# Performance work log

Hardware: AMD Instinct MI355X
Metric: run time of the kernel (lower is better)

## Reference

```python
import jax, jax.numpy as jnp
import numpy as np

TEMP = 0.3  # softmax temperature used in load-balance loss


def setup_inputs() -> dict:
    key = jax.random.key(0)
    k1, k2 = jax.random.split(key)
    num_tokens, d_model, num_expert = 16384, 4096, 128
    inp = jax.random.normal(k1, (num_tokens, d_model), dtype=jnp.float32)
    wg = jax.random.normal(k2, (num_expert, d_model), dtype=jnp.float32) * (1.0 / np.sqrt(d_model))
    return {"inp": inp, "wg": wg, "top_k": 2}


def reference(inp, wg, top_k):
    # Gate logits: [T, E] = [T, D] @ [D, E]
    logits = jnp.einsum("td,ed->te", inp, wg)
    # Top-k selection + softmax over the k selected logits
    top_vals, top_idx = jax.lax.top_k(logits, top_k)  # [T, k]
    gate_score = jax.nn.softmax(top_vals, axis=-1)    # [T, k]
    # Load-balance loss (stored as self.loss in torch; returned here)
    T, E = logits.shape
    probs = jax.nn.softmax(logits / TEMP, axis=-1)    # [T, E]
    mask = jax.nn.one_hot(top_idx[:, 0], E, dtype=probs.dtype) * (E / T)
    me = jnp.sum(probs, axis=0)                       # [E]
    ce = jnp.sum(mask, axis=0)                        # [E]
    loss = jnp.sum(me * ce) / T
    return top_idx, gate_score, loss
```

## Files before the change

### kernel.cpp

```cpp
#include <hip/hip_runtime.h>

typedef _Float16 half8 __attribute__((ext_vector_type(8)));
typedef float floatx4 __attribute__((ext_vector_type(4)));

#define NTOK 16384
#define DM   4096
#define NE   128
#define MT   32
#define BK   64
#define KSPLIT 2
#define KHALF (DM / KSPLIT)
#define NITER (KHALF / BK)
#define NBLK_MAIN (NTOK / MT * KSPLIT)
#define ET   64
#define NBLK_EPI (NTOK / ET)
#define TEMP 0.3f
#define CSTRIDE 528
#define ABUF (8 * CSTRIDE)
#define BUFSZ (2 * ABUF)

__global__ void pack_b_kernel(const float* __restrict__ wg, _Float16* __restrict__ Bp) {
    int gtid = blockIdx.x * blockDim.x + threadIdx.x;
    int l  = gtid & 63;
    int tg = gtid >> 6;
    int g  = tg & 7;
    int kc = tg >> 3;
    const float* src = wg + (size_t)(g * 16 + (l & 15)) * DM + kc * 32 + (l >> 4) * 8;
    float4 v0 = *(const float4*)src;
    float4 v1 = *(const float4*)(src + 4);
    float f[8] = {v0.x, v0.y, v0.z, v0.w, v1.x, v1.y, v1.z, v1.w};
    half8 h1, h2;
#pragma unroll
    for (int j = 0; j < 8; j++) {
        h1[j] = (_Float16)f[j];
        h2[j] = (_Float16)((f[j] - (float)h1[j]) * 2048.0f);
    }
    char* dst = (char*)Bp + (size_t)tg * 2048 + l * 16;
    *(half8*)dst = h1;
    *(half8*)(dst + 1024) = h2;
}

__device__ __forceinline__ void stage_write(unsigned char* base, unsigned off,
                                            float4 v0, float4 v1) {
    float f[8] = {v0.x, v0.y, v0.z, v0.w, v1.x, v1.y, v1.z, v1.w};
    half8 h1, h2;
#pragma unroll
    for (int j = 0; j < 8; j++) {
        h1[j] = (_Float16)f[j];
        h2[j] = (_Float16)((f[j] - (float)h1[j]) * 2048.0f);
    }
    *(half8*)(base + off) = h1;
    *(half8*)(base + ABUF + off) = h2;
}

__launch_bounds__(256, 4)
__global__ void moe_gemm_kernel(const float* __restrict__ A,
                                const _Float16* __restrict__ Bp,
                                float* __restrict__ part) {
    __shared__ __align__(16) unsigned char smem[2 * BUFSZ];
    const int tid  = threadIdx.x;
    const int wave = tid >> 6;
    const int lane = tid & 63;
    const int quad = lane >> 4;
    const int lrow = lane & 15;
    const int half = blockIdx.x & 1;
    const int tok0 = (blockIdx.x >> 1) * MT;

    const int srow = tid >> 3;
    const int schunk = tid & 7;
    const float* aptr = A + (size_t)(tok0 + srow) * DM + half * KHALF + schunk * 8;
    const unsigned swoff = schunk * CSTRIDE + srow * 16;
    const unsigned aroff = quad * CSTRIDE + lrow * 16;

    const char* bB = (const char*)Bp + (size_t)half * (1u << 20) + (wave * 2) * 2048 + lane * 16;

    floatx4 accm[2][2], accc[2][2];
#pragma unroll
    for (int r = 0; r < 2; r++)
#pragma unroll
        for (int c = 0; c < 2; c++) {
            accm[r][c] = (floatx4){0.f, 0.f, 0.f, 0.f};
            accc[r][c] = (floatx4){0.f, 0.f, 0.f, 0.f};
        }

    {
        float4 v0 = *(const float4*)aptr;
        float4 v1 = *(const float4*)(aptr + 4);
        stage_write(smem, swoff, v0, v1);
    }
    __syncthreads();

    for (int it = 0; it < NITER; ++it) {
        float4 n0, n1;
        if (it < NITER - 1) {
            const float* p = aptr + (it + 1) * BK;
            n0 = *(const float4*)p;
            n1 = *(const float4*)(p + 4);
        }
        unsigned char* cb = smem + (it & 1) * BUFSZ;
        const char* bit = bB + (size_t)it * 32768;

#pragma unroll
        for (int ks = 0; ks < 2; ++ks) {
            half8 b1f[2], b2f[2], a1[2], a2[2];
#pragma unroll
            for (int c = 0; c < 2; c++) {
                b1f[c] = *(const half8*)(bit + ks * 16384 + c * 2048);
                b2f[c] = *(const half8*)(bit + ks * 16384 + c * 2048 + 1024);
            }
#pragma unroll
            for (int r = 0; r < 2; r++) {
                a1[r] = *(const half8*)(cb + ks * 2112 + r * 256 + aroff);
                a2[r] = *(const half8*)(cb + ABUF + ks * 2112 + r * 256 + aroff);
            }
#pragma unroll
            for (int r = 0; r < 2; r++)
#pragma unroll
                for (int c = 0; c < 2; c++) {
                    accm[r][c] = __builtin_amdgcn_mfma_f32_16x16x32_f16(a1[r], b1f[c], accm[r][c], 0, 0, 0);
                    accc[r][c] = __builtin_amdgcn_mfma_f32_16x16x32_f16(a1[r], b2f[c], accc[r][c], 0, 0, 0);
                    accc[r][c] = __builtin_amdgcn_mfma_f32_16x16x32_f16(a2[r], b1f[c], accc[r][c], 0, 0, 0);
                }
        }
        if (it < NITER - 1)
            stage_write(smem + ((it + 1) & 1) * BUFSZ, swoff, n0, n1);
        __syncthreads();
    }

    float* pbase = part + (size_t)half * NTOK * NE;
#pragma unroll
    for (int r = 0; r < 2; r++)
#pragma unroll
        for (int c = 0; c < 2; c++) {
            floatx4 v;
#pragma unroll
            for (int g = 0; g < 4; g++)
                v[g] = accm[r][c][g] + accc[r][c][g] * (1.0f / 2048.0f);
            int e = wave * 32 + c * 16 + lrow;
            int t = tok0 + r * 16 + quad * 4;
            *(floatx4*)(pbase + (size_t)e * NTOK + t) = v;
        }
}

__global__ void topk_kernel(const float* __restrict__ part,
                            float* __restrict__ out,
                            float* __restrict__ me_part,
                            float* __restrict__ ce_part) {
    __shared__ float LG[NE * 68];
    __shared__ float tmax[ET], tscale[ET];
    __shared__ int hist[NE];
    const int tid = threadIdx.x;
    const int t0  = blockIdx.x * ET;
    const float* p0 = part;
    const float* p1 = part + (size_t)NTOK * NE;

    {
        const int q = tid & 3;
#pragma unroll
        for (int pass = 0; pass < 2; pass++) {
            int e = (tid >> 2) + pass * 64;
            const float* r0 = p0 + (size_t)e * NTOK + t0 + q * 16;
            const float* r1 = p1 + (size_t)e * NTOK + t0 + q * 16;
            float* dst = LG + e * 68 + q * 16;
#pragma unroll
            for (int j = 0; j < 16; j += 4) {
                float4 a = *(const float4*)(r0 + j);
                float4 b = *(const float4*)(r1 + j);
                float4 s = {a.x + b.x, a.y + b.y, a.z + b.z, a.w + b.w};
                *(float4*)(dst + j) = s;
            }
        }
    }
    if (tid < NE) hist[tid] = 0;
    __syncthreads();

    if (tid < ET) {
        const int t = tid;
        float m1 = -1e30f, m2 = -1e30f;
        int i1 = 0, i2 = 0;
        for (int e = 0; e < NE; e++) {
            float v = LG[e * 68 + t];
            if (v > m1) { m2 = m1; i2 = i1; m1 = v; i1 = e; }
            else if (v > m2) { m2 = v; i2 = e; }
        }
        float s = 0.f;
        for (int e = 0; e < NE; e++)
            s += __expf((LG[e * 68 + t] - m1) * (1.0f / TEMP));
        tmax[t] = m1;
        tscale[t] = 1.0f / s;
        atomicAdd(&hist[i1], 1);

        const int tg = t0 + t;
        out[tg * 2 + 0] = (float)i1;
        out[tg * 2 + 1] = (float)i2;
        float d = __expf(m2 - m1);
        float g1 = 1.0f / (1.0f + d);
        out[2 * NTOK + tg * 2 + 0] = g1;
        out[2 * NTOK + tg * 2 + 1] = d * g1;
    }
    __syncthreads();

    if (tid < NE) {
        const int e = tid;
        float s = 0.f;
        for (int t = 0; t < ET; t++)
            s += __expf((LG[e * 68 + t] - tmax[t]) * (1.0f / TEMP)) * tscale[t];
        me_part[blockIdx.x * NE + e] = s;
        ce_part[blockIdx.x * NE + e] = (float)hist[e];
    }
}

__global__ void finalize_kernel(const float* __restrict__ mp, const float* __restrict__ cp,
                                float* __restrict__ out) {
    __shared__ float red[2 * 8 * 128];
    __shared__ float wsum[2];
    const int tid = threadIdx.x;
    const int e = tid & 127, seg = tid >> 7;
    float sm = 0.f, sc = 0.f;
    for (int b = seg; b < NBLK_EPI; b += 8) {
        sm += mp[b * NE + e];
        sc += cp[b * NE + e];
    }
    red[seg * 128 + e] = sm;
    red[1024 + seg * 128 + e] = sc;
    __syncthreads();
    if (tid < 128) {
        float me = 0.f, ce = 0.f;
#pragma unroll
        for (int s = 0; s < 8; s++) {
            me += red[s * 128 + tid];
            ce += red[1024 + s * 128 + tid];
        }
        ce *= (float)NE / (float)NTOK;
        float v = me * ce;
#pragma unroll
        for (int off = 32; off; off >>= 1) v += __shfl_down(v, off);
        if ((tid & 63) == 0) wsum[tid >> 6] = v;
    }
    __syncthreads();
    if (tid == 0) out[4 * NTOK] = (wsum[0] + wsum[1]) / (float)NTOK;
}

extern "C" void kernel_launch(void* const* d_in, const int* in_sizes, int n_in,
                              void* d_out, int out_size, void* d_ws, size_t ws_size,
                              hipStream_t stream) {
    (void)in_sizes; (void)n_in; (void)out_size; (void)ws_size;
    const float* inp = (const float*)d_in[0];
    const float* wg  = (const float*)d_in[1];
    float* out = (float*)d_out;

    _Float16* Bp = (_Float16*)d_ws;
    float* part = (float*)((char*)d_ws + (2u << 20));
    float* mp = (float*)((char*)d_ws + (18u << 20));
    float* cp = mp + NBLK_EPI * NE;

    pack_b_kernel<<<256, 256, 0, stream>>>(wg, Bp);
    moe_gemm_kernel<<<NBLK_MAIN, 256, 0, stream>>>(inp, Bp, part);
    topk_kernel<<<NBLK_EPI, 256, 0, stream>>>(part, out, mp, cp);
    finalize_kernel<<<1, 1024, 0, stream>>>(mp, cp, out);
}
```

Baseline: 427.4 us.

## Fuse top-k and loss epilogue into GEMM, drop split-K and partial buffers

Removes the K-split so each block computes full logits for 32 tokens, then writes the logits to shared memory and runs the top-k, gate softmax and per-expert probability sums in the same kernel. Per-expert me/ce sums go to a small global buffer through atomics, and finalize just reduces 128 values. This drops the 16MB partial-logit round trip and a kernel launch. In exchange the grid has half as many blocks with twice the K loop each, occupancy is reduced to 2 blocks per CU, and there is global atomic contention plus a memset.

```diff
diff --git a/kernel.cpp b/kernel.cpp
--- a/kernel.cpp
+++ b/kernel.cpp
@@ -8,16 +8,13 @@
 #define NE   128
 #define MT   32
 #define BK   64
-#define KSPLIT 2
-#define KHALF (DM / KSPLIT)
-#define NITER (KHALF / BK)
-#define NBLK_MAIN (NTOK / MT * KSPLIT)
-#define ET   64
-#define NBLK_EPI (NTOK / ET)
+#define NITER (DM / BK)
+#define NBLK (NTOK / MT)
 #define TEMP 0.3f
 #define CSTRIDE 528
 #define ABUF (8 * CSTRIDE)
 #define BUFSZ (2 * ABUF)
+#define LSTRIDE 33
 
 __global__ void pack_b_kernel(const float* __restrict__ wg, _Float16* __restrict__ Bp) {
     int gtid = blockIdx.x * blockDim.x + threadIdx.x;
@@ -53,26 +50,28 @@
     *(half8*)(base + ABUF + off) = h2;
 }
 
-__launch_bounds__(256, 4)
-__global__ void moe_gemm_kernel(const float* __restrict__ A,
-                                const _Float16* __restrict__ Bp,
-                                float* __restrict__ part) {
+__launch_bounds__(256, 2)
+__global__ void moe_fused_kernel(const float* __restrict__ A,
+                                 const _Float16* __restrict__ Bp,
+                                 float* __restrict__ out,
+                                 float* __restrict__ mece) {
     __shared__ __align__(16) unsigned char smem[2 * BUFSZ];
+    __shared__ float tmax[MT], tscale[MT];
+    float* LG = (float*)smem;
     const int tid  = threadIdx.x;
     const int wave = tid >> 6;
     const int lane = tid & 63;
     const int quad = lane >> 4;
     const int lrow = lane & 15;
-    const int half = blockIdx.x & 1;
-    const int tok0 = (blockIdx.x >> 1) * MT;
+    const int tok0 = blockIdx.x * MT;
 
     const int srow = tid >> 3;
     const int schunk = tid & 7;
-    const float* aptr = A + (size_t)(tok0 + srow) * DM + half * KHALF + schunk * 8;
+    const float* aptr = A + (size_t)(tok0 + srow) * DM + schunk * 8;
     const unsigned swoff = schunk * CSTRIDE + srow * 16;
     const unsigned aroff = quad * CSTRIDE + lrow * 16;
 
-    const char* bB = (const char*)Bp + (size_t)half * (1u << 20) + (wave * 2) * 2048 + lane * 16;
+    const char* bB = (const char*)Bp + (wave * 2) * 2048 + lane * 16;
 
     floatx4 accm[2][2], accc[2][2];
 #pragma unroll
@@ -127,118 +126,64 @@
         __syncthreads();
     }
 
-    float* pbase = part + (size_t)half * NTOK * NE;
 #pragma unroll
     for (int r = 0; r < 2; r++)
 #pragma unroll
         for (int c = 0; c < 2; c++) {
-            floatx4 v;
+            const int e  = wave * 32 + c * 16 + lrow;
+            const int tt = r * 16 + quad * 4;
 #pragma unroll
             for (int g = 0; g < 4; g++)
-                v[g] = accm[r][c][g] + accc[r][c][g] * (1.0f / 2048.0f);
-            int e = wave * 32 + c * 16 + lrow;
-            int t = tok0 + r * 16 + quad * 4;
-            *(floatx4*)(pbase + (size_t)e * NTOK + t) = v;
-        }
-}
-
-__global__ void topk_kernel(const float* __restrict__ part,
-                            float* __restrict__ out,
-                            float* __restrict__ me_part,
-                            float* __restrict__ ce_part) {
-    __shared__ float LG[NE * 68];
-    __shared__ float tmax[ET], tscale[ET];
-    __shared__ int hist[NE];
-    const int tid = threadIdx.x;
-    const int t0  = blockIdx.x * ET;
-    const float* p0 = part;
-    const float* p1 = part + (size_t)NTOK * NE;
-
-    {
-        const int q = tid & 3;
-#pragma unroll
-        for (int pass = 0; pass < 2; pass++) {
-            int e = (tid >> 2) + pass * 64;
-            const float* r0 = p0 + (size_t)e * NTOK + t0 + q * 16;
-            const float* r1 = p1 + (size_t)e * NTOK + t0 + q * 16;
-            float* dst = LG + e * 68 + q * 16;
-#pragma unroll
-            for (int j = 0; j < 16; j += 4) {
-                float4 a = *(const float4*)(r0 + j);
-                float4 b = *(const float4*)(r1 + j);
-                float4 s = {a.x + b.x, a.y + b.y, a.z + b.z, a.w + b.w};
-                *(float4*)(dst + j) = s;
-            }
-        }
-    }
-    if (tid < NE) hist[tid] = 0;
-    __syncthreads();
-
-    if (tid < ET) {
+                LG[e * LSTRIDE + tt + g] = accm[r][c][g] + accc[r][c][g] * (1.0f / 2048.0f);
+        }
+    __syncthreads();
+
+    if (tid < MT) {
         const int t = tid;
         float m1 = -1e30f, m2 = -1e30f;
         int i1 = 0, i2 = 0;
         for (int e = 0; e < NE; e++) {
-            float v = LG[e * 68 + t];
+            float v = LG[e * LSTRIDE + t];
             if (v > m1) { m2 = m1; i2 = i1; m1 = v; i1 = e; }
             else if (v > m2) { m2 = v; i2 = e; }
         }
         float s = 0.f;
         for (int e = 0; e < NE; e++)
-            s += __expf((LG[e * 68 + t] - m1) * (1.0f / TEMP));
+            s += __expf((LG[e * LSTRIDE + t] - m1) * (1.0f / TEMP));
         tmax[t] = m1;
         tscale[t] = 1.0f / s;
-        atomicAdd(&hist[i1], 1);
-
-        const int tg = t0 + t;
+
+        const int tg = tok0 + t;
         out[tg * 2 + 0] = (float)i1;
         out[tg * 2 + 1] = (float)i2;
         float d = __expf(m2 - m1);
         float g1 = 1.0f / (1.0f + d);
         out[2 * NTOK + tg * 2 + 0] = g1;
         out[2 * NTOK + tg * 2 + 1] = d * g1;
+
+        atomicAdd(&mece[NE + i1], 1.0f);
     }
     __syncthreads();
 
     if (tid < NE) {
         const int e = tid;
         float s = 0.f;
-        for (int t = 0; t < ET; t++)
-            s += __expf((LG[e * 68 + t] - tmax[t]) * (1.0f / TEMP)) * tscale[t];
-        me_part[blockIdx.x * NE + e] = s;
-        ce_part[blockIdx.x * NE + e] = (float)hist[e];
-    }
-}
-
-__global__ void finalize_kernel(const float* __restrict__ mp, const float* __restrict__ cp,
-                                float* __restrict__ out) {
-    __shared__ float red[2 * 8 * 128];
-    __shared__ float wsum[2];
+#pragma unroll
+        for (int t = 0; t < MT; t++)
+            s += __expf((LG[e * LSTRIDE + t] - tmax[t]) * (1.0f / TEMP)) * tscale[t];
+        atomicAdd(&mece[e], s);
+    }
+}
+
+__global__ void finalize_kernel(const float* __restrict__ mece, float* __restrict__ out) {
+    __shared__ float w2[2];
     const int tid = threadIdx.x;
-    const int e = tid & 127, seg = tid >> 7;
-    float sm = 0.f, sc = 0.f;
-    for (int b = seg; b < NBLK_EPI; b += 8) {
-        sm += mp[b * NE + e];
-        sc += cp[b * NE + e];
-    }
-    red[seg * 128 + e] = sm;
-    red[1024 + seg * 128 + e] = sc;
-    __syncthreads();
-    if (tid < 128) {
-        float me = 0.f, ce = 0.f;
-#pragma unroll
-        for (int s = 0; s < 8; s++) {
-            me += red[s * 128 + tid];
-            ce += red[1024 + s * 128 + tid];
-        }
-        ce *= (float)NE / (float)NTOK;
-        float v = me * ce;
-#pragma unroll
-        for (int off = 32; off; off >>= 1) v += __shfl_down(v, off);
-        if ((tid & 63) == 0) wsum[tid >> 6] = v;
-    }
-    __syncthreads();
-    if (tid == 0) out[4 * NTOK] = (wsum[0] + wsum[1]) / (float)NTOK;
+    float v = mece[tid] * mece[NE + tid] * ((float)NE / (float)NTOK);
+#pragma unroll
+    for (int off = 32; off; off >>= 1) v += __shfl_down(v, off);
+    if ((tid & 63) == 0) w2[tid >> 6] = v;
+    __syncthreads();
+    if (tid == 0) out[4 * NTOK] = (w2[0] + w2[1]) / (float)NTOK;
 }
 
 extern "C" void kernel_launch(void* const* d_in, const int* in_sizes, int n_in,
@@ -250,12 +195,10 @@
     float* out = (float*)d_out;
 
     _Float16* Bp = (_Float16*)d_ws;
-    float* part = (float*)((char*)d_ws + (2u << 20));
-    float* mp = (float*)((char*)d_ws + (18u << 20));
-    float* cp = mp + NBLK_EPI * NE;
-
+    float* mece  = (float*)((char*)d_ws + (2u << 20));
+
+    hipMemsetAsync(mece, 0, 2 * NE * sizeof(float), stream);
     pack_b_kernel<<<256, 256, 0, stream>>>(wg, Bp);
-    moe_gemm_kernel<<<NBLK_MAIN, 256, 0, stream>>>(inp, Bp, part);
-    topk_kernel<<<NBLK_EPI, 256, 0, stream>>>(part, out, mp, cp);
-    finalize_kernel<<<1, 1024, 0, stream>>>(mp, cp, out);
-}
+    moe_fused_kernel<<<NBLK, 256, 0, stream>>>(inp, Bp, out, mece);
+    finalize_kernel<<<1, NE, 0, stream>>>(mece, out);
+}
```

Measured after the change: 465.9 us. 1.09x slower.
